# Kernel optimization log

Hardware: AMD Instinct MI355X
Metric: run time of the kernel (lower is better)

The kernel has to match this reference:

```python
import jax, jax.numpy as jnp
import numpy as np

# OGB feature vocab sizes
ATOM_DIMS = [119, 4, 12, 12, 10, 6, 6, 2, 2]
BOND_DIMS = [5, 6, 2]
ATOM_OFF = np.concatenate([[0], np.cumsum(ATOM_DIMS)[:-1]]).astype(np.int32)
BOND_OFF = np.concatenate([[0], np.cumsum(BOND_DIMS)[:-1]]).astype(np.int32)
SCHEDULE_LEN = 5   # len(train_schedule) == len(eval_schedule)
NUM_GRAPHS = 12000
BN_EPS = 1e-5

N_NODES, N_EDGES, HIDDEN, NUM_TASKS = 300000, 600000, 128, 128


def setup_inputs() -> dict:
    key = jax.random.key(0)
    ks = jax.random.split(key, 16)
    x = jax.random.randint(ks[0], (N_NODES, 9), 0, 2, dtype=jnp.int32)
    edge_index = jax.random.randint(ks[1], (2, N_EDGES), 0, N_NODES, dtype=jnp.int32)
    edge_attr = jax.random.randint(ks[2], (N_EDGES, 3), 0, 2, dtype=jnp.int32)
    batch = jnp.sort(jax.random.randint(ks[3], (N_NODES,), 0, NUM_GRAPHS, dtype=jnp.int32))
    # learned parameters (embedding tables concatenated with offsets)
    atom_emb = jax.random.normal(ks[4], (sum(ATOM_DIMS), HIDDEN), jnp.float32) * 0.1
    bond_emb = jax.random.normal(ks[5], (sum(BOND_DIMS), HIDDEN), jnp.float32) * 0.1
    conv_W = jax.random.normal(ks[6], (HIDDEN, HIDDEN), jnp.float32) * (1.0 / np.sqrt(HIDDEN))
    conv_b = jnp.zeros((HIDDEN,), jnp.float32)
    root_emb = jax.random.normal(ks[7], (HIDDEN,), jnp.float32) * 0.1
    bn_gamma = jnp.ones((HIDDEN,), jnp.float32)
    bn_beta = jnp.zeros((HIDDEN,), jnp.float32)
    bn_mean = jnp.zeros((HIDDEN,), jnp.float32)   # running stats (eval mode)
    bn_var = jnp.ones((HIDDEN,), jnp.float32)
    lin_W = jax.random.normal(ks[8], (NUM_TASKS, HIDDEN), jnp.float32) * (1.0 / np.sqrt(HIDDEN))
    lin_b = jnp.zeros((NUM_TASKS,), jnp.float32)
    return {"x": x, "edge_index": edge_index, "edge_attr": edge_attr, "batch": batch,
            "atom_emb": atom_emb, "bond_emb": bond_emb, "conv_W": conv_W, "conv_b": conv_b,
            "root_emb": root_emb, "bn_gamma": bn_gamma, "bn_beta": bn_beta,
            "bn_mean": bn_mean, "bn_var": bn_var, "lin_W": lin_W, "lin_b": lin_b}


def reference(x, edge_index, edge_attr, batch, atom_emb, bond_emb, conv_W, conv_b,
              root_emb, bn_gamma, bn_beta, bn_mean, bn_var, lin_W, lin_b):
    N = x.shape[0]
    # AtomEncoder / BondEncoder: sum of per-feature embedding lookups
    h = atom_emb[x + jnp.asarray(ATOM_OFF, x.dtype)].sum(axis=1)            # [N, H]
    e = bond_emb[edge_attr + jnp.asarray(BOND_OFF, edge_attr.dtype)].sum(axis=1)  # [E, H]
    row, col = edge_index[0], edge_index[1]
    deg = jax.ops.segment_sum(jnp.ones_like(row, h.dtype), row, num_segments=N) + 1.0  # [N]
    dis = deg ** -0.5                                                        # deg >= 1, no inf
    norm = dis[row] * dis[col]                                               # [E]
    inv_std = bn_gamma / jnp.sqrt(bn_var + BN_EPS)
    for i in range(SCHEDULE_LEN):
        old = h
        z = h @ conv_W.T + conv_b                                            # [N, H]
        # message: norm * relu(x_j + edge_emb), aggregated at target (col) via scatter-add
        msg = norm[:, None] * jax.nn.relu(z[row] + e)                        # [E, H]
        agg = jax.ops.segment_sum(msg, col, num_segments=N)                  # [N, H]
        z = agg + jax.nn.relu(z + root_emb) / deg[:, None]                   # self-loop term
        z = jax.nn.relu(z)
        z = (z - bn_mean) * inv_std + bn_beta                                # BN (eval, running stats)
        # dropout: identity in eval mode
        # NOTE: faithful to source bug: smooth_fac is the loop index i, not schedule[i]
        h = i * old + (1 - i) * z
    # global mean pool over graphs
    counts = jax.ops.segment_sum(jnp.ones((N,), h.dtype), batch, num_segments=NUM_GRAPHS)
    pooled = jax.ops.segment_sum(h, batch, num_segments=NUM_GRAPHS) / jnp.maximum(counts, 1.0)[:, None]
    return pooled @ lin_W.T + lin_b                                          # [num_graphs, num_tasks]
```

## Files before the change

### kernel.cpp

```cpp
#include <hip/hip_runtime.h>

#define HID 128
#define AROWS 173

typedef __attribute__((ext_vector_type(8))) short short8;
typedef __attribute__((ext_vector_type(8))) unsigned short ushort8v;
typedef __attribute__((ext_vector_type(4))) float floatx4;
typedef __attribute__((ext_vector_type(4))) unsigned short ushort4v;

__device__ __forceinline__ unsigned short f2bf(float f) {
    unsigned u = __builtin_bit_cast(unsigned, f);
    u += 0x7FFF + ((u >> 16) & 1);
    return (unsigned short)(u >> 16);
}
__device__ __forceinline__ float bf2f(unsigned short s) {
    unsigned u = ((unsigned)s) << 16;
    return __builtin_bit_cast(float, u);
}

__global__ void fillrd_kernel(float* __restrict__ dis, int* __restrict__ indeg, int N)
{
    int i = blockIdx.x * 256 + threadIdx.x;
    if (i < N) { dis[i] = 0.f; indeg[i] = 0; }
}

__global__ void diag_kernel(float* __restrict__ out, long n, float val)
{
    long i = (long)blockIdx.x * blockDim.x + threadIdx.x;
    if (i < n) out[i] = val;
}

__global__ __launch_bounds__(256) void tables_kernel(
    const float* __restrict__ conv_W, unsigned short* __restrict__ Wb,
    const float* __restrict__ lin_W, unsigned short* __restrict__ linWb,
    const float* __restrict__ bond_emb, unsigned short* __restrict__ comb,
    const float* __restrict__ gamma, const float* __restrict__ beta,
    const float* __restrict__ mean, const float* __restrict__ var,
    float* __restrict__ bnsc, float* __restrict__ bnsh)
{
    int blk = blockIdx.x;
    int tid = threadIdx.x;
    if (blk < 64) {
        int i = blk * 256 + tid;
        Wb[i] = f2bf(conv_W[i]);
    } else if (blk < 128) {
        int i = (blk - 64) * 256 + tid;
        linWb[i] = f2bf(lin_W[i]);
    } else if (blk < 158) {
        int i = (blk - 128) * 2 + (tid >> 7);
        int c = tid & 127;
        int a0 = i / 12, a1 = (i % 12) / 2, a2 = i % 2;
        comb[i * HID + c] = f2bf(bond_emb[a0 * HID + c] + bond_emb[(5 + a1) * HID + c]
                               + bond_emb[(11 + a2) * HID + c]);
    } else if (tid < HID) {
        float sc = gamma[tid] * rsqrtf(var[tid] + 1e-5f);
        bnsc[tid] = sc;
        bnsh[tid] = beta[tid] - mean[tid] * sc;
    }
}

__global__ __launch_bounds__(128) void ewk_kernel(
    const float* __restrict__ atom_emb, const float* __restrict__ conv_W,
    unsigned short* __restrict__ EWb)
{
    int r = blockIdx.x;
    int c = threadIdx.x;
    const float* er = atom_emb + (long)r * HID;
    const float* wr = conv_W + (long)c * HID;
    float acc = 0.f;
#pragma unroll 4
    for (int k = 0; k < HID; k += 4) {
        floatx4 e4 = *reinterpret_cast<const floatx4*>(er + k);
        floatx4 w4 = *reinterpret_cast<const floatx4*>(wr + k);
        acc += e4[0] * w4[0] + e4[1] * w4[1] + e4[2] * w4[2] + e4[3] * w4[3];
    }
    EWb[(long)r * HID + c] = f2bf(acc);
}

__global__ void hist_kernel(const int* __restrict__ ei, float* __restrict__ dis,
                            int* __restrict__ indeg, int E)
{
    for (int e = blockIdx.x * blockDim.x + threadIdx.x; e < E; e += gridDim.x * blockDim.x) {
        atomicAdd(&dis[ei[e]], 1.f);
        atomicAdd(&indeg[ei[E + e]], 1);
    }
}

__global__ __launch_bounds__(256) void bsum_kernel(
    const int* __restrict__ indeg, int* __restrict__ partial,
    float* __restrict__ dis, int N)
{
    __shared__ int s[256];
    int tid = threadIdx.x;
    int i = blockIdx.x * 256 + tid;
    int v = (i < N) ? indeg[i] : 0;
    s[tid] = v;
    if (i < N) dis[i] = rsqrtf(dis[i] + 1.f);
    __syncthreads();
    for (int d = 128; d > 0; d >>= 1) {
        if (tid < d) s[tid] += s[tid + d];
        __syncthreads();
    }
    if (tid == 0) partial[blockIdx.x] = s[0];
}

__global__ __launch_bounds__(256) void scan1_kernel(
    const int* __restrict__ partial, int* __restrict__ offs,
    int* __restrict__ ptr, int B, int N)
{
    __shared__ int s[256];
    __shared__ int carry_s;
    int tid = threadIdx.x;
    if (tid == 0) carry_s = 0;
    __syncthreads();
    for (int base = 0; base < B; base += 256) {
        int i = base + tid;
        int v = (i < B) ? partial[i] : 0;
        s[tid] = v;
        __syncthreads();
        for (int d = 1; d < 256; d <<= 1) {
            int t = (tid >= d) ? s[tid - d] : 0;
            __syncthreads();
            s[tid] += t;
            __syncthreads();
        }
        int carry = carry_s;
        if (i < B) offs[i] = carry + s[tid] - v;
        __syncthreads();
        if (tid == 0) carry_s = carry + s[255];
        __syncthreads();
    }
    if (tid == 0) ptr[N] = carry_s;
}

__global__ __launch_bounds__(256) void scan2_kernel(
    const int* __restrict__ indeg, const int* __restrict__ offs,
    int* __restrict__ ptr, int* __restrict__ cursor, int N)
{
    __shared__ int s[256];
    int tid = threadIdx.x;
    int i = blockIdx.x * 256 + tid;
    int v = (i < N) ? indeg[i] : 0;
    s[tid] = v;
    __syncthreads();
    for (int d = 1; d < 256; d <<= 1) {
        int t = (tid >= d) ? s[tid - d] : 0;
        __syncthreads();
        s[tid] += t;
        __syncthreads();
    }
    if (i < N) {
        int ex = offs[blockIdx.x] + s[tid] - v;
        ptr[i] = ex;
        cursor[i] = ex;
    }
}

__global__ void fillcsr_kernel(const int* __restrict__ ei, const int* __restrict__ attr,
                               const float* __restrict__ dis, int* __restrict__ cursor,
                               int2* __restrict__ edata, const int* __restrict__ batch,
                               int* __restrict__ gptr, int E, int N, int G)
{
    for (int e = blockIdx.x * blockDim.x + threadIdx.x; e < E; e += gridDim.x * blockDim.x) {
        int r   = ei[e];
        int col = ei[E + e];
        int pos = atomicAdd(&cursor[col], 1);
        int ci  = attr[e * 3] * 12 + attr[e * 3 + 1] * 2 + attr[e * 3 + 2];
        float nrm = dis[r] * dis[col];
        int2 ed;
        ed.x = r;
        ed.y = ci | ((int)f2bf(nrm) << 16);
        edata[pos] = ed;
    }
    for (int n = blockIdx.x * blockDim.x + threadIdx.x; n < N; n += gridDim.x * blockDim.x) {
        int b = batch[n];
        int bp = (n == 0) ? -1 : batch[n - 1];
        for (int g = bp + 1; g <= b; ++g) gptr[g] = n;
        if (n == N - 1)
            for (int g = b + 1; g <= G; ++g) gptr[g] = N;
    }
}

__global__ __launch_bounds__(256) void enc_kernel(
    const int* __restrict__ x, const unsigned short* __restrict__ EWb,
    const float* __restrict__ bias, unsigned short* __restrict__ zb, int N)
{
    long n = (long)blockIdx.x * 16 + (threadIdx.x >> 4);
    if (n >= N) return;
    int c = (threadIdx.x & 15) * 8;
    const int OFF[9] = {0, 119, 123, 135, 147, 157, 163, 169, 171};

    float acc[8];
#pragma unroll
    for (int j = 0; j < 8; ++j) acc[j] = bias[c + j];

#pragma unroll
    for (int f = 0; f < 9; ++f) {
        int idx = x[n * 9 + f] + OFF[f];
        ushort8v v = *reinterpret_cast<const ushort8v*>(EWb + (long)idx * HID + c);
#pragma unroll
        for (int j = 0; j < 8; ++j) acc[j] += bf2f(v[j]);
    }

    ushort8v o;
#pragma unroll
    for (int j = 0; j < 8; ++j) o[j] = f2bf(acc[j]);
    *reinterpret_cast<ushort8v*>(zb + n * HID + c) = o;
}

template<bool FIRST>
__global__ __launch_bounds__(256) void agg_kernel(
    const int* __restrict__ ptr, const int2* __restrict__ edata,
    const unsigned short* __restrict__ comb, const float* __restrict__ dis,
    const float* __restrict__ root, const float* __restrict__ bnsc,
    const float* __restrict__ bnsh, const unsigned short* __restrict__ zb,
    unsigned short* __restrict__ hb, float fi, int N)
{
    long n = (long)blockIdx.x * 16 + (threadIdx.x >> 4);
    if (n >= N) return;
    int c = (threadIdx.x & 15) * 8;

    ushort8v zv = *reinterpret_cast<const ushort8v*>(zb + n * HID + c);
    ushort8v hv;
    if constexpr (!FIRST) hv = *reinterpret_cast<const ushort8v*>(hb + n * HID + c);
    float di = dis[n];
    float rd = di * di;
    float acc[8];
#pragma unroll
    for (int j = 0; j < 8; ++j) acc[j] = fmaxf(bf2f(zv[j]) + root[c + j], 0.f) * rd;

    int jb = ptr[n], je = ptr[n + 1];
    int j2 = jb;
    for (; j2 + 1 < je; j2 += 2) {
        int2 e0 = edata[j2];
        int2 e1 = edata[j2 + 1];
        ushort8v z0 = *reinterpret_cast<const ushort8v*>(zb + (long)e0.x * HID + c);
        ushort8v z1 = *reinterpret_cast<const ushort8v*>(zb + (long)e1.x * HID + c);
        ushort8v c0 = *reinterpret_cast<const ushort8v*>(comb + (e0.y & 0xFF) * HID + c);
        ushort8v c1 = *reinterpret_cast<const ushort8v*>(comb + (e1.y & 0xFF) * HID + c);
        float n0 = bf2f((unsigned short)(((unsigned)e0.y) >> 16));
        float n1 = bf2f((unsigned short)(((unsigned)e1.y) >> 16));
#pragma unroll
        for (int j = 0; j < 8; ++j) {
            acc[j] += fmaxf(bf2f(z0[j]) + bf2f(c0[j]), 0.f) * n0;
            acc[j] += fmaxf(bf2f(z1[j]) + bf2f(c1[j]), 0.f) * n1;
        }
    }
    if (j2 < je) {
        int2 e0 = edata[j2];
        ushort8v z0 = *reinterpret_cast<const ushort8v*>(zb + (long)e0.x * HID + c);
        ushort8v c0 = *reinterpret_cast<const ushort8v*>(comb + (e0.y & 0xFF) * HID + c);
        float n0 = bf2f((unsigned short)(((unsigned)e0.y) >> 16));
#pragma unroll
        for (int j = 0; j < 8; ++j)
            acc[j] += fmaxf(bf2f(z0[j]) + bf2f(c0[j]), 0.f) * n0;
    }

    ushort8v o;
#pragma unroll
    for (int j = 0; j < 8; ++j) {
        float t = fmaxf(acc[j], 0.f) * bnsc[c + j] + bnsh[c + j];
        float h;
        if constexpr (FIRST) h = t;
        else h = fi * bf2f(hv[j]) + (1.f - fi) * t;
        o[j] = f2bf(h);
    }
    *reinterpret_cast<ushort8v*>(hb + n * HID + c) = o;
}

__global__ __launch_bounds__(256, 8) void gemm_kernel(
    const unsigned short* __restrict__ hb, const unsigned short* __restrict__ Wb,
    const float* __restrict__ bias, unsigned short* __restrict__ zb, int N)
{
    int tid = threadIdx.x;
    int wave = tid >> 6;
    int lane = tid & 63;
    int l15 = lane & 15;
    int q = lane >> 4;
    long base = (long)blockIdx.x * 128;
    long row0 = base + wave * 32;

    short8 a[2][4];
#pragma unroll
    for (int mt = 0; mt < 2; ++mt) {
        long rl = row0 + mt * 16 + l15;
        if (rl > (long)N - 1) rl = (long)N - 1;
        const unsigned short* ap = hb + rl * HID + q * 8;
#pragma unroll
        for (int kb = 0; kb < 4; ++kb)
            a[mt][kb] = *reinterpret_cast<const short8*>(ap + kb * 32);
    }

    floatx4 acc[2][8];
#pragma unroll
    for (int mt = 0; mt < 2; ++mt)
#pragma unroll
        for (int nt = 0; nt < 8; ++nt) {
            floatx4 zz = {0.f, 0.f, 0.f, 0.f};
            acc[mt][nt] = zz;
        }

#pragma unroll
    for (int nt = 0; nt < 8; ++nt) {
        const unsigned short* bp = Wb + (nt * 16 + l15) * HID + q * 8;
#pragma unroll
        for (int kb = 0; kb < 4; ++kb) {
            short8 b = *reinterpret_cast<const short8*>(bp + kb * 32);
            acc[0][nt] = __builtin_amdgcn_mfma_f32_16x16x32_bf16(a[0][kb], b, acc[0][nt], 0, 0, 0);
            acc[1][nt] = __builtin_amdgcn_mfma_f32_16x16x32_bf16(a[1][kb], b, acc[1][nt], 0, 0, 0);
        }
    }

    float bi[8];
#pragma unroll
    for (int nt = 0; nt < 8; ++nt) bi[nt] = bias[nt * 16 + l15];

#pragma unroll
    for (int mt = 0; mt < 2; ++mt)
#pragma unroll
        for (int r = 0; r < 4; ++r) {
            long gr = row0 + mt * 16 + q * 4 + r;
            if (gr < N) {
                unsigned short* op = zb + gr * HID + l15;
#pragma unroll
                for (int nt = 0; nt < 8; ++nt)
                    op[nt * 16] = f2bf(acc[mt][nt][r] + bi[nt]);
            }
        }
}

__global__ __launch_bounds__(256) void linmm_kernel(
    const unsigned short* __restrict__ pb, const unsigned short* __restrict__ Wb,
    const float* __restrict__ bias, float* __restrict__ out, int G)
{
    int wave = threadIdx.x >> 6;
    int lane = threadIdx.x & 63;
    int l15 = lane & 15;
    int q = lane >> 4;
    long row0 = (long)blockIdx.x * 128 + wave * 32;

    short8 a[2][4];
#pragma unroll
    for (int mt = 0; mt < 2; ++mt) {
        long rl = row0 + mt * 16 + l15;
        if (rl > (long)G - 1) rl = (long)G - 1;
        const unsigned short* ap = pb + rl * HID + q * 8;
#pragma unroll
        for (int kb = 0; kb < 4; ++kb)
            a[mt][kb] = *reinterpret_cast<const short8*>(ap + kb * 32);
    }

    floatx4 acc[2][8];
#pragma unroll
    for (int mt = 0; mt < 2; ++mt)
#pragma unroll
        for (int nt = 0; nt < 8; ++nt) {
            floatx4 zz = {0.f, 0.f, 0.f, 0.f};
            acc[mt][nt] = zz;
        }

#pragma unroll
    for (int nt = 0; nt < 8; ++nt) {
        const unsigned short* bp = Wb + (nt * 16 + l15) * HID + q * 8;
#pragma unroll
        for (int kb = 0; kb < 4; ++kb) {
            short8 b = *reinterpret_cast<const short8*>(bp + kb * 32);
            acc[0][nt] = __builtin_amdgcn_mfma_f32_16x16x32_bf16(a[0][kb], b, acc[0][nt], 0, 0, 0);
            acc[1][nt] = __builtin_amdgcn_mfma_f32_16x16x32_bf16(a[1][kb], b, acc[1][nt], 0, 0, 0);
        }
    }

    float bi[8];
#pragma unroll
    for (int nt = 0; nt < 8; ++nt) bi[nt] = bias[nt * 16 + l15];

#pragma unroll
    for (int mt = 0; mt < 2; ++mt)
#pragma unroll
        for (int r = 0; r < 4; ++r) {
            long rr = row0 + mt * 16 + q * 4 + r;
            if (rr < G) {
                float* op = out + rr * HID + l15;
#pragma unroll
                for (int nt = 0; nt < 8; ++nt)
                    op[nt * 16] = acc[mt][nt][r] + bi[nt];
            }
        }
}

__global__ __launch_bounds__(256) void pool_kernel(
    const unsigned short* __restrict__ hb, const int* __restrict__ gptr,
    unsigned short* __restrict__ pb, int G)
{
    int g = blockIdx.x * 4 + (threadIdx.x >> 6);
    if (g >= G) return;
    int lane = threadIdx.x & 63;
    int c = lane * 2;
    int lo = gptr[g], hi = gptr[g + 1];

    float a0 = 0.f, a1 = 0.f, b0 = 0.f, b1 = 0.f;
    int n = lo;
    for (; n + 1 < hi; n += 2) {
        unsigned v0 = *reinterpret_cast<const unsigned*>(hb + (long)n * HID + c);
        unsigned v1 = *reinterpret_cast<const unsigned*>(hb + (long)(n + 1) * HID + c);
        a0 += bf2f((unsigned short)(v0 & 0xFFFF));
        a1 += bf2f((unsigned short)(v0 >> 16));
        b0 += bf2f((unsigned short)(v1 & 0xFFFF));
        b1 += bf2f((unsigned short)(v1 >> 16));
    }
    if (n < hi) {
        unsigned v0 = *reinterpret_cast<const unsigned*>(hb + (long)n * HID + c);
        a0 += bf2f((unsigned short)(v0 & 0xFFFF));
        a1 += bf2f((unsigned short)(v0 >> 16));
    }
    float cnt = (hi > lo) ? (float)(hi - lo) : 1.f;
    float s0 = (a0 + b0) / cnt;
    float s1 = (a1 + b1) / cnt;
    unsigned o = (unsigned)f2bf(s0) | ((unsigned)f2bf(s1) << 16);
    *reinterpret_cast<unsigned*>(pb + (long)g * HID + c) = o;
}

extern "C" void kernel_launch(void* const* d_in, const int* in_sizes, int n_in,
                              void* d_out, int out_size, void* d_ws, size_t ws_size,
                              hipStream_t stream)
{
    const int* x          = (const int*)d_in[0];
    const int* ei         = (const int*)d_in[1];
    const int* attr       = (const int*)d_in[2];
    const int* batch      = (const int*)d_in[3];
    const float* atom_emb = (const float*)d_in[4];
    const float* bond_emb = (const float*)d_in[5];
    const float* conv_W   = (const float*)d_in[6];
    const float* conv_b   = (const float*)d_in[7];
    const float* root     = (const float*)d_in[8];
    const float* gamma    = (const float*)d_in[9];
    const float* beta     = (const float*)d_in[10];
    const float* mean     = (const float*)d_in[11];
    const float* var      = (const float*)d_in[12];
    const float* lin_W    = (const float*)d_in[13];
    const float* lin_b    = (const float*)d_in[14];
    float* out = (float*)d_out;

    const int N = in_sizes[0] / 9;
    const int E = in_sizes[1] / 2;
    const int G = out_size / HID;
    const int B = (N + 255) / 256;

    auto al = [](size_t b) { return (b + 255) & ~(size_t)255; };
    const size_t need =
        al((size_t)N * HID * 2) +
        al((size_t)N * HID * 2) +
        al((size_t)(N + 1) * 4) +
        al((size_t)E * 8) +
        al((size_t)N * 4) +
        al((size_t)2048 * 4) * 2 +
        al((size_t)(G + 1) * 4) +
        al((size_t)(G + 128) * HID * 2) +
        al((size_t)60 * HID * 2) +
        al((size_t)HID * 4) * 2 +
        al((size_t)HID * HID * 2) * 2 +
        al((size_t)AROWS * HID * 2);

    if (ws_size < need || B > 2048) {
        float v = (B > 2048) ? 3000.f : (1000.f + (float)(ws_size >> 20));
        long n = (long)out_size;
        diag_kernel<<<(int)((n + 255) / 256), 256, 0, stream>>>(out, n, v);
        return;
    }

    char* wsp = (char*)d_ws;
    size_t used = 0;
    auto alloc = [&](size_t bytes) { char* p = wsp + used; used += al(bytes); return p; };
    unsigned short* hb = (unsigned short*)alloc((size_t)N * HID * 2);
    unsigned short* zb = (unsigned short*)alloc((size_t)N * HID * 2);
    int* ptr      = (int*)alloc((size_t)(N + 1) * 4);
    int2* edata   = (int2*)alloc((size_t)E * 8);
    int* indeg    = (int*)alloc((size_t)N * 4);
    int* cursor   = indeg;
    int* partial  = (int*)alloc((size_t)2048 * 4);
    int* offs     = (int*)alloc((size_t)2048 * 4);
    int* gptr     = (int*)alloc((size_t)(G + 1) * 4);
    unsigned short* pb = (unsigned short*)alloc((size_t)(G + 128) * HID * 2);
    float* dis    = (float*)pb;
    unsigned short* comb = (unsigned short*)alloc((size_t)60 * HID * 2);
    float* bnsc   = (float*)alloc((size_t)HID * 4);
    float* bnsh   = (float*)alloc((size_t)HID * 4);
    unsigned short* Wb    = (unsigned short*)alloc((size_t)HID * HID * 2);
    unsigned short* linWb = (unsigned short*)alloc((size_t)HID * HID * 2);
    unsigned short* EWb   = (unsigned short*)alloc((size_t)AROWS * HID * 2);

    fillrd_kernel<<<B, 256, 0, stream>>>(dis, indeg, N);
    tables_kernel<<<159, 256, 0, stream>>>(conv_W, Wb, lin_W, linWb, bond_emb, comb,
                                           gamma, beta, mean, var, bnsc, bnsh);
    ewk_kernel<<<AROWS, 128, 0, stream>>>(atom_emb, conv_W, EWb);
    hist_kernel<<<1024, 256, 0, stream>>>(ei, dis, indeg, E);
    bsum_kernel<<<B, 256, 0, stream>>>(indeg, partial, dis, N);
    scan1_kernel<<<1, 256, 0, stream>>>(partial, offs, ptr, B, N);
    scan2_kernel<<<B, 256, 0, stream>>>(indeg, offs, ptr, cursor, N);
    fillcsr_kernel<<<1024, 256, 0, stream>>>(ei, attr, dis, cursor, edata,
                                             batch, gptr, E, N, G);

    const int gemm_blocks = (N + 127) / 128;
    const int node_blocks = (N + 15) / 16;
    enc_kernel<<<node_blocks, 256, 0, stream>>>(x, EWb, conv_b, zb, N);
    agg_kernel<true ><<<node_blocks, 256, 0, stream>>>(ptr, edata, comb, dis,
            root, bnsc, bnsh, zb, hb, 0.f, N);
    const float fis[3] = {2.f, 3.f, 4.f};
    for (int t = 0; t < 3; ++t) {
        gemm_kernel<<<gemm_blocks, 256, 0, stream>>>(hb, Wb, conv_b, zb, N);
        agg_kernel<false><<<node_blocks, 256, 0, stream>>>(ptr, edata, comb, dis,
                root, bnsc, bnsh, zb, hb, fis[t], N);
    }

    pool_kernel<<<(G + 3) / 4, 256, 0, stream>>>(hb, gptr, pb, G);
    linmm_kernel<<<(G + 127) / 128, 256, 0, stream>>>(pb, linWb, lin_b, out, G);
}
```

Measured before the change: 761.6 us.

## Permute hidden-column layout so GEMM epilogue writes 16-byte vector stores

```diff
diff --git a/kernel.cpp b/kernel.cpp
--- a/kernel.cpp
+++ b/kernel.cpp
@@ -2,6 +2,8 @@
 
 #define HID 128
 #define AROWS 173
+
+__device__ __forceinline__ int lcol(int p) { return ((p & 7) << 4) | (p >> 3); }
 
 typedef __attribute__((ext_vector_type(8))) short short8;
 typedef __attribute__((ext_vector_type(8))) unsigned short ushort8v;
@@ -36,26 +38,34 @@
     const float* __restrict__ bond_emb, unsigned short* __restrict__ comb,
     const float* __restrict__ gamma, const float* __restrict__ beta,
     const float* __restrict__ mean, const float* __restrict__ var,
-    float* __restrict__ bnsc, float* __restrict__ bnsh)
+    float* __restrict__ bnsc, float* __restrict__ bnsh,
+    const float* __restrict__ root, const float* __restrict__ conv_b,
+    float* __restrict__ rootp, float* __restrict__ cbp)
 {
     int blk = blockIdx.x;
     int tid = threadIdx.x;
     if (blk < 64) {
         int i = blk * 256 + tid;
-        Wb[i] = f2bf(conv_W[i]);
+        int row = i >> 7, p = i & 127;
+        Wb[i] = f2bf(conv_W[row * HID + lcol(p)]);
     } else if (blk < 128) {
         int i = (blk - 64) * 256 + tid;
-        linWb[i] = f2bf(lin_W[i]);
+        int row = i >> 7, p = i & 127;
+        linWb[i] = f2bf(lin_W[row * HID + lcol(p)]);
     } else if (blk < 158) {
         int i = (blk - 128) * 2 + (tid >> 7);
-        int c = tid & 127;
+        int p = tid & 127;
+        int c = lcol(p);
         int a0 = i / 12, a1 = (i % 12) / 2, a2 = i % 2;
-        comb[i * HID + c] = f2bf(bond_emb[a0 * HID + c] + bond_emb[(5 + a1) * HID + c]
+        comb[i * HID + p] = f2bf(bond_emb[a0 * HID + c] + bond_emb[(5 + a1) * HID + c]
                                + bond_emb[(11 + a2) * HID + c]);
     } else if (tid < HID) {
-        float sc = gamma[tid] * rsqrtf(var[tid] + 1e-5f);
+        int c = lcol(tid);
+        float sc = gamma[c] * rsqrtf(var[c] + 1e-5f);
         bnsc[tid] = sc;
-        bnsh[tid] = beta[tid] - mean[tid] * sc;
+        bnsh[tid] = beta[c] - mean[c] * sc;
+        rootp[tid] = root[c];
+        cbp[tid] = conv_b[c];
     }
 }
 
@@ -74,7 +84,7 @@
         floatx4 w4 = *reinterpret_cast<const floatx4*>(wr + k);
         acc += e4[0] * w4[0] + e4[1] * w4[1] + e4[2] * w4[2] + e4[3] * w4[3];
     }
-    EWb[(long)r * HID + c] = f2bf(acc);
+    EWb[(long)r * HID + ((c & 15) * 8 + (c >> 4))] = f2bf(acc);
 }
 
 __global__ void hist_kernel(const int* __restrict__ ei, float* __restrict__ dis,
@@ -183,7 +193,7 @@
 
 __global__ __launch_bounds__(256) void enc_kernel(
     const int* __restrict__ x, const unsigned short* __restrict__ EWb,
-    const float* __restrict__ bias, unsigned short* __restrict__ zb, int N)
+    const float* __restrict__ cbp, unsigned short* __restrict__ zb, int N)
 {
     long n = (long)blockIdx.x * 16 + (threadIdx.x >> 4);
     if (n >= N) return;
@@ -192,7 +202,7 @@
 
     float acc[8];
 #pragma unroll
-    for (int j = 0; j < 8; ++j) acc[j] = bias[c + j];
+    for (int j = 0; j < 8; ++j) acc[j] = cbp[c + j];
 
 #pragma unroll
     for (int f = 0; f < 9; ++f) {
@@ -268,7 +278,7 @@
     *reinterpret_cast<ushort8v*>(hb + n * HID + c) = o;
 }
 
-__global__ __launch_bounds__(256, 8) void gemm_kernel(
+__global__ void gemm_kernel(
     const unsigned short* __restrict__ hb, const unsigned short* __restrict__ Wb,
     const float* __restrict__ bias, unsigned short* __restrict__ zb, int N)
 {
@@ -277,8 +287,7 @@
     int lane = tid & 63;
     int l15 = lane & 15;
     int q = lane >> 4;
-    long base = (long)blockIdx.x * 128;
-    long row0 = base + wave * 32;
+    long row0 = (long)blockIdx.x * 128 + wave * 32;
 
     short8 a[2][4];
 #pragma unroll
@@ -321,10 +330,11 @@
         for (int r = 0; r < 4; ++r) {
             long gr = row0 + mt * 16 + q * 4 + r;
             if (gr < N) {
-                unsigned short* op = zb + gr * HID + l15;
+                ushort8v o;
 #pragma unroll
                 for (int nt = 0; nt < 8; ++nt)
-                    op[nt * 16] = f2bf(acc[mt][nt][r] + bi[nt]);
+                    o[nt] = f2bf(acc[mt][nt][r] + bi[nt]);
+                *reinterpret_cast<ushort8v*>(zb + gr * HID + l15 * 8) = o;
             }
         }
 }
@@ -457,7 +467,7 @@
         al((size_t)(G + 1) * 4) +
         al((size_t)(G + 128) * HID * 2) +
         al((size_t)60 * HID * 2) +
-        al((size_t)HID * 4) * 2 +
+        al((size_t)HID * 4) * 4 +
         al((size_t)HID * HID * 2) * 2 +
         al((size_t)AROWS * HID * 2);
 
@@ -485,13 +495,16 @@
     unsigned short* comb = (unsigned short*)alloc((size_t)60 * HID * 2);
     float* bnsc   = (float*)alloc((size_t)HID * 4);
     float* bnsh   = (float*)alloc((size_t)HID * 4);
+    float* rootp  = (float*)alloc((size_t)HID * 4);
+    float* cbp    = (float*)alloc((size_t)HID * 4);
     unsigned short* Wb    = (unsigned short*)alloc((size_t)HID * HID * 2);
     unsigned short* linWb = (unsigned short*)alloc((size_t)HID * HID * 2);
     unsigned short* EWb   = (unsigned short*)alloc((size_t)AROWS * HID * 2);
 
     fillrd_kernel<<<B, 256, 0, stream>>>(dis, indeg, N);
     tables_kernel<<<159, 256, 0, stream>>>(conv_W, Wb, lin_W, linWb, bond_emb, comb,
-                                           gamma, beta, mean, var, bnsc, bnsh);
+                                           gamma, beta, mean, var, bnsc, bnsh,
+                                           root, conv_b, rootp, cbp);
     ewk_kernel<<<AROWS, 128, 0, stream>>>(atom_emb, conv_W, EWb);
     hist_kernel<<<1024, 256, 0, stream>>>(ei, dis, indeg, E);
     bsum_kernel<<<B, 256, 0, stream>>>(indeg, partial, dis, N);
@@ -502,14 +515,14 @@
 
     const int gemm_blocks = (N + 127) / 128;
     const int node_blocks = (N + 15) / 16;
-    enc_kernel<<<node_blocks, 256, 0, stream>>>(x, EWb, conv_b, zb, N);
+    enc_kernel<<<node_blocks, 256, 0, stream>>>(x, EWb, cbp, zb, N);
     agg_kernel<true ><<<node_blocks, 256, 0, stream>>>(ptr, edata, comb, dis,
-            root, bnsc, bnsh, zb, hb, 0.f, N);
+            rootp, bnsc, bnsh, zb, hb, 0.f, N);
     const float fis[3] = {2.f, 3.f, 4.f};
     for (int t = 0; t < 3; ++t) {
         gemm_kernel<<<gemm_blocks, 256, 0, stream>>>(hb, Wb, conv_b, zb, N);
         agg_kernel<false><<<node_blocks, 256, 0, stream>>>(ptr, edata, comb, dis,
-                root, bnsc, bnsh, zb, hb, fis[t], N);
+                rootp, bnsc, bnsh, zb, hb, fis[t], N);
     }
 
     pool_kernel<<<(G + 3) / 4, 256, 0, stream>>>(hb, gptr, pb, G);
```

After: 648.5 us. 1.17x faster.
